# Kernel tuning notes

Measured on AMD Instinct MI355X. Metric: run time of the kernel, lower is better.

Reference implementation:

```python
import jax, jax.numpy as jnp
import numpy as np


def setup_inputs() -> dict:
    key = jax.random.key(0)
    kx, kr, kq, kk, kv = jax.random.split(key, 5)
    B, T, N, C = 4, 8, 2048, 128
    w_scale = 1.0 / np.sqrt(C)  # keep logits in a sane range
    return {
        "x": jax.random.normal(kx, (B, T, N, C), dtype=jnp.float32),
        "residual_source": jax.random.normal(kr, (B, N, C), dtype=jnp.float32),
        "Wq": jax.random.normal(kq, (C, C), dtype=jnp.float32) * w_scale,
        "Wk": jax.random.normal(kk, (C, C), dtype=jnp.float32) * w_scale,
        "Wv": jax.random.normal(kv, (C, C), dtype=jnp.float32) * w_scale,
    }


def reference(x, residual_source, Wq, Wk, Wv):
    # x: [B, T, N, C]; residual_source: [B, M, C] (expanded along T in the
    # original via unsqueeze+expand; here we exploit broadcasting instead of
    # materializing the [B, T, M, C] copy -- same math, k/v identical per T).
    q = jnp.einsum("btnc,cd->btnd", x, Wq)               # [B, T, N, D]
    k = jnp.einsum("bmc,cd->bmd", residual_source, Wk)   # [B, M, D]
    v = jnp.einsum("bmc,cd->bmd", residual_source, Wv)   # [B, M, D]
    # Unscaled attention, exactly as in the original (no 1/sqrt(d)).
    affinities = jnp.einsum("btnd,bmd->btnm", q, k)       # [B, T, N, M]
    attn = jax.nn.softmax(affinities, axis=-1)
    residual = jnp.einsum("btnm,bmd->btnd", attn, v)      # [B, T, N, D]
    return x + residual
```

## Files before the change

kernel.cpp:

```cpp
#include <hip/hip_runtime.h>


#define Bn 4
#define Tn 8
#define Nn 2048
#define Cn 128
#define Mn 2048
#define KVB 32
#define NT 64
#define QROWS 128
#define NQT (Nn / QROWS)

typedef __attribute__((ext_vector_type(4))) float f32x4;
typedef __attribute__((ext_vector_type(8))) _Float16 f16x8;
typedef __attribute__((address_space(3))) unsigned char lds_uc;
typedef const __attribute__((address_space(1))) unsigned char glb_uc;

__device__ __forceinline__ unsigned short f2h(float f) {
  _Float16 h = (_Float16)f;
  return __builtin_bit_cast(unsigned short, h);
}
__device__ __forceinline__ unsigned int pk2(float a, float b) {
  auto v = __builtin_amdgcn_cvt_pkrtz(a, b);
  return __builtin_bit_cast(unsigned int, v);
}
__device__ __forceinline__ f16x8 lds_read8(const unsigned char* base, int row,
                                           int colByte) {
  int byte = row * 256 + (colByte ^ ((row & 7) << 4));
  return *(const f16x8*)(base + byte);
}
__device__ __forceinline__ f16x8 lds_read8v(const unsigned char* base, int row,
                                            int colByte) {
  int byte = row * 64 + (colByte ^ ((row & 3) << 4));
  return *(const f16x8*)(base + byte);
}
__device__ __forceinline__ void gld16(const void* g, void* l) {
  __builtin_amdgcn_global_load_lds((glb_uc*)g, (lds_uc*)l, 16, 0, 0);
}

__global__ __launch_bounds__(256) void proj_kv_kernel(
    const float* __restrict__ rs, const float* __restrict__ Wk,
    const float* __restrict__ Wv, unsigned short* __restrict__ k_ws,
    unsigned short* __restrict__ vt_ws) {
  __shared__ unsigned char smem[48 * 1024];
  unsigned char* rsh = smem;
  unsigned char* wt = smem + 16 * 1024;

  const int bid = blockIdx.x;
  const int b = bid >> 5;
  const int kt64 = bid & 31;
  const int m0 = kt64 << 6;
  const int tid = threadIdx.x;
  const int wv = tid >> 6, lane = tid & 63;

  {
    const float4* g = (const float4*)(rs + ((size_t)b * Mn + m0) * Cn);
#pragma unroll
    for (int i = 0; i < 8; ++i) {
      int f = tid + i * 256;
      int row = f >> 5, c4 = f & 31;
      float4 v = g[f];
      int byte = row * 256 + ((c4 * 8) ^ ((row & 7) << 4));
      *(ushort4*)(rsh + byte) =
          make_ushort4(f2h(v.x), f2h(v.y), f2h(v.z), f2h(v.w));
    }
  }

#define STAGE_WT(Wp)                                                          \
  {                                                                           \
    const float4* g = (const float4*)(Wp);                                    \
    _Pragma("unroll") for (int i = 0; i < 16; ++i) {                          \
      int f = tid + i * 256;                                                  \
      int cc = f >> 5, d0 = (f & 31) * 4;                                     \
      float4 v = g[f];                                                        \
      float vv[4] = {v.x, v.y, v.z, v.w};                                     \
      _Pragma("unroll") for (int j = 0; j < 4; ++j) {                         \
        int row = d0 + j;                                                     \
        int byte = row * 256 + ((cc * 2) ^ ((row & 7) << 4));                 \
        *(unsigned short*)(wt + byte) = f2h(vv[j]);                           \
      }                                                                       \
    }                                                                         \
  }

  STAGE_WT(Wk);
  __syncthreads();

  const int arow = wv * 16 + (lane & 15);
  f16x8 ah[4];
#pragma unroll
  for (int ks = 0; ks < 4; ++ks)
    ah[ks] = lds_read8(rsh, arow, (lane >> 4) * 16 + ks * 64);

  f32x4 acc[8];
#pragma unroll
  for (int df = 0; df < 8; ++df) acc[df] = (f32x4)(0.0f);
#pragma unroll
  for (int ks = 0; ks < 4; ++ks)
#pragma unroll
    for (int df = 0; df < 8; ++df) {
      f16x8 bf = lds_read8(wt, df * 16 + (lane & 15), (lane >> 4) * 16 + ks * 64);
      acc[df] = __builtin_amdgcn_mfma_f32_16x16x32_f16(ah[ks], bf, acc[df], 0, 0, 0);
    }
  {
    unsigned char* kb = (unsigned char*)k_ws;
#pragma unroll
    for (int df = 0; df < 8; ++df)
#pragma unroll
      for (int r = 0; r < 4; ++r) {
        int row = wv * 16 + (lane >> 4) * 4 + r;
        int dcol = df * 16 + (lane & 15);
        size_t tile = (size_t)b * NT + (m0 >> 5) + (row >> 5);
        size_t byte = tile * 8192 + (row & 31) * 256 +
                      ((dcol * 2) ^ ((row & 7) << 4));
        *(unsigned short*)(kb + byte) = f2h(acc[df][r]);
      }
  }
  __syncthreads();

  STAGE_WT(Wv);
  __syncthreads();
#pragma unroll
  for (int df = 0; df < 8; ++df) acc[df] = (f32x4)(0.0f);
#pragma unroll
  for (int ks = 0; ks < 4; ++ks)
#pragma unroll
    for (int df = 0; df < 8; ++df) {
      f16x8 bf = lds_read8(wt, df * 16 + (lane & 15), (lane >> 4) * 16 + ks * 64);
      acc[df] = __builtin_amdgcn_mfma_f32_16x16x32_f16(ah[ks], bf, acc[df], 0, 0, 0);
    }
  {
    unsigned char* vb = (unsigned char*)vt_ws;
#pragma unroll
    for (int df = 0; df < 8; ++df)
#pragma unroll
      for (int r = 0; r < 4; ++r) {
        int row = wv * 16 + (lane >> 4) * 4 + r;
        int dcol = df * 16 + (lane & 15);
        size_t tile = (size_t)b * NT + (m0 >> 5) + (row >> 5);
        size_t byte = tile * 8192 + dcol * 64 +
                      (((row & 31) * 2) ^ ((dcol & 3) << 4));
        *(unsigned short*)(vb + byte) = f2h(acc[df][r]);
      }
  }
#undef STAGE_WT
}

__global__ __launch_bounds__(256, 2) void attn_kernel(
    const float* __restrict__ x, const float* __restrict__ Wq,
    const unsigned short* __restrict__ k_ws,
    const unsigned short* __restrict__ vt_ws, float* __restrict__ out) {
  __shared__ unsigned char smem[64 * 1024];

  const int bx = blockIdx.x;
  const int wb = ((bx & 7) << 6) | (bx >> 3);
  const int b = wb >> 7;
  const int t_ = (wb >> 4) & 7;
  const int n0 = (wb & 15) * QROWS;
  const int tid = threadIdx.x;
  const int wv = tid >> 6, lane = tid & 63;
  const int c = lane & 15, g = lane >> 4;

  const float* xg = x + (((size_t)b * Tn + t_) * Nn + n0) * Cn;
  unsigned char* xa = smem;
  unsigned char* wqb = smem + 32 * 1024;
  unsigned char* pb = smem + 48 * 1024 + wv * 2048;

  {
    const float4* gp = (const float4*)xg;
#pragma unroll
    for (int ii = 0; ii < 16; ++ii) {
      int f = tid + ii * 256;
      int row = f >> 5, c4 = f & 31;
      float4 v = gp[f];
      int byte = row * 256 + ((c4 * 8) ^ ((row & 7) << 4));
      *(ushort4*)(xa + byte) =
          make_ushort4(f2h(v.x), f2h(v.y), f2h(v.z), f2h(v.w));
    }
  }
  {
    const float4* gp = (const float4*)Wq;
#pragma unroll
    for (int ii = 0; ii < 16; ++ii) {
      int f = tid + ii * 256;
      int cc = f >> 5, d0 = (f & 31) * 4;
      float4 v = gp[f];
      float vv[4] = {v.x, v.y, v.z, v.w};
#pragma unroll
      for (int j = 0; j < 4; ++j) {
        int row = d0 + j;
        int byte = row * 256 + ((cc * 2) ^ ((row & 7) << 4));
        *(unsigned short*)(wqb + byte) = f2h(vv[j]);
      }
    }
  }
  __syncthreads();

  f32x4 qacc[2][8];
#pragma unroll
  for (int rb = 0; rb < 2; ++rb)
#pragma unroll
    for (int df = 0; df < 8; ++df) qacc[rb][df] = (f32x4)(0.0f);
  {
    f16x8 xf[2][4];
#pragma unroll
    for (int rb = 0; rb < 2; ++rb)
#pragma unroll
      for (int ks = 0; ks < 4; ++ks)
        xf[rb][ks] = lds_read8(xa, wv * 32 + rb * 16 + c, g * 16 + ks * 64);
#pragma unroll
    for (int ks = 0; ks < 4; ++ks)
#pragma unroll
      for (int df = 0; df < 8; ++df) {
        f16x8 bf = lds_read8(wqb, df * 16 + c, g * 16 + ks * 64);
        qacc[0][df] = __builtin_amdgcn_mfma_f32_16x16x32_f16(xf[0][ks], bf, qacc[0][df], 0, 0, 0);
        qacc[1][df] = __builtin_amdgcn_mfma_f32_16x16x32_f16(xf[1][ks], bf, qacc[1][df], 0, 0, 0);
      }
  }
  const float LOG2E = 1.4426950408889634f;
#pragma unroll
  for (int rb = 0; rb < 2; ++rb)
#pragma unroll
    for (int df = 0; df < 8; ++df)
#pragma unroll
      for (int r = 0; r < 4; ++r) {
        int row = wv * 32 + rb * 16 + g * 4 + r;
        int col = df * 16 + c;
        int byte = row * 256 + ((col * 2) ^ ((row & 7) << 4));
        *(unsigned short*)(xa + byte) = f2h(qacc[rb][df][r] * LOG2E);
      }
  f16x8 qf[2][4];
#pragma unroll
  for (int rb = 0; rb < 2; ++rb)
#pragma unroll
    for (int ks = 0; ks < 4; ++ks)
      qf[rb][ks] = lds_read8(xa, wv * 32 + rb * 16 + c, g * 16 + ks * 64);
  __syncthreads();

  f32x4 o[2][8];
#pragma unroll
  for (int rb = 0; rb < 2; ++rb)
#pragma unroll
    for (int df = 0; df < 8; ++df) o[rb][df] = (f32x4)(0.0f);
  float mrow[2] = {-INFINITY, -INFINITY};
  float lrow[2] = {0.f, 0.f};

  const unsigned char* khg = (const unsigned char*)k_ws + (size_t)b * NT * 8192;
  const unsigned char* vtg = (const unsigned char*)vt_ws + (size_t)b * NT * 8192;

  auto stageK = [&](int t) {
    const unsigned char* s = khg + (size_t)t * 8192 + tid * 16;
    unsigned char* d = smem + (t & 1) * 8192 + tid * 16;
    gld16(s, d);
    gld16(s + 4096, d + 4096);
  };
  auto stageV = [&](int t) {
    const unsigned char* s = vtg + (size_t)t * 8192 + tid * 16;
    unsigned char* d = smem + 16 * 1024 + (t & 3) * 8192 + tid * 16;
    gld16(s, d);
    gld16(s + 4096, d + 4096);
  };

  stageK(0);
  stageV(0);
  stageV(1);
  asm volatile("s_waitcnt vmcnt(2)" ::: "memory");
  __builtin_amdgcn_s_barrier();

  f16x8 pa[2];
#pragma unroll 1
  for (int t = 0; t < NT; ++t) {
    unsigned char* kb = smem + (t & 1) * 8192;
    unsigned char* vbp = smem + 16 * 1024 + ((t - 1) & 3) * 8192;

    f32x4 st[2][2];
#pragma unroll
    for (int rb = 0; rb < 2; ++rb)
#pragma unroll
      for (int kvb = 0; kvb < 2; ++kvb) st[rb][kvb] = (f32x4)(0.0f);
    __builtin_amdgcn_s_setprio(1);
#pragma unroll
    for (int ks = 0; ks < 4; ++ks)
#pragma unroll
      for (int kvb = 0; kvb < 2; ++kvb) {
        f16x8 kf = lds_read8(kb, kvb * 16 + c, g * 16 + ks * 64);
        st[0][kvb] = __builtin_amdgcn_mfma_f32_16x16x32_f16(kf, qf[0][ks], st[0][kvb], 0, 0, 0);
        st[1][kvb] = __builtin_amdgcn_mfma_f32_16x16x32_f16(kf, qf[1][ks], st[1][kvb], 0, 0, 0);
      }
    if (t > 0) {
#pragma unroll
      for (int df = 0; df < 8; ++df) {
        f16x8 vf = lds_read8v(vbp, df * 16 + c, g * 16);
        o[0][df] = __builtin_amdgcn_mfma_f32_16x16x32_f16(vf, pa[0], o[0][df], 0, 0, 0);
        o[1][df] = __builtin_amdgcn_mfma_f32_16x16x32_f16(vf, pa[1], o[1][df], 0, 0, 0);
      }
    }
    __builtin_amdgcn_s_setprio(0);

    if (t + 1 < NT) stageK(t + 1);
    if (t + 2 < NT) stageV(t + 2);

#pragma unroll
    for (int rb = 0; rb < 2; ++rb) {
      float tm = st[rb][0][0];
#pragma unroll
      for (int kvb = 0; kvb < 2; ++kvb)
#pragma unroll
        for (int r = 0; r < 4; ++r) tm = fmaxf(tm, st[rb][kvb][r]);
      if (__any(tm > mrow[rb] + 8.f)) {
        tm = fmaxf(tm, __shfl_xor(tm, 16));
        tm = fmaxf(tm, __shfl_xor(tm, 32));
        float newm = fmaxf(mrow[rb], tm);
        float scl = exp2f(mrow[rb] - newm);
#pragma unroll
        for (int df = 0; df < 8; ++df) o[rb][df] *= scl;
        lrow[rb] *= scl;
        mrow[rb] = newm;
      }
      float mn = mrow[rb];
      float ps = 0.f;
#pragma unroll
      for (int kvb = 0; kvb < 2; ++kvb) {
        float p0 = exp2f(st[rb][kvb][0] - mn);
        float p1 = exp2f(st[rb][kvb][1] - mn);
        float p2 = exp2f(st[rb][kvb][2] - mn);
        float p3 = exp2f(st[rb][kvb][3] - mn);
        ps += (p0 + p1) + (p2 + p3);
        int kv2 = kvb * 32 + g * 8;
        int base = rb * 1024 + c * 64;
        int swz = (c & 3) << 4;
        *(unsigned int*)(pb + base + (kv2 ^ swz)) = pk2(p0, p1);
        *(unsigned int*)(pb + base + ((kv2 + 4) ^ swz)) = pk2(p2, p3);
      }
      lrow[rb] += ps;
    }

    pa[0] = lds_read8v(pb, c, g * 16);
    pa[1] = lds_read8v(pb + 1024, c, g * 16);

    if (t < NT - 1) {
      if (t < NT - 2)
        asm volatile("s_waitcnt vmcnt(2)" ::: "memory");
      else
        asm volatile("s_waitcnt vmcnt(0)" ::: "memory");
      __builtin_amdgcn_s_barrier();
    }
  }
  {
    unsigned char* vbp = smem + 16 * 1024 + ((NT - 1) & 3) * 8192;
#pragma unroll
    for (int df = 0; df < 8; ++df) {
      f16x8 vf = lds_read8v(vbp, df * 16 + c, g * 16);
      o[0][df] = __builtin_amdgcn_mfma_f32_16x16x32_f16(vf, pa[0], o[0][df], 0, 0, 0);
      o[1][df] = __builtin_amdgcn_mfma_f32_16x16x32_f16(vf, pa[1], o[1][df], 0, 0, 0);
    }
  }
  __syncthreads();

#pragma unroll
  for (int rb = 0; rb < 2; ++rb) {
    lrow[rb] += __shfl_xor(lrow[rb], 16);
    lrow[rb] += __shfl_xor(lrow[rb], 32);
  }
  float inv[2] = {1.0f / lrow[0], 1.0f / lrow[1]};
#pragma unroll
  for (int rb = 0; rb < 2; ++rb)
#pragma unroll
    for (int df = 0; df < 8; ++df)
#pragma unroll
      for (int tq = 0; tq < 2; ++tq) {
        int d0 = df * 16 + g * 4 + tq * 2;
        int row = wv * 32 + rb * 16 + c;
        int byte = row * 256 + ((d0 * 2) ^ ((row & 7) << 4));
        *(unsigned int*)(smem + byte) =
            pk2(o[rb][df][2 * tq] * inv[rb], o[rb][df][2 * tq + 1] * inv[rb]);
      }
  __syncthreads();
  {
    const float4* xg4 = (const float4*)xg;
    float4* og4 = (float4*)(out + (((size_t)b * Tn + t_) * Nn + n0) * Cn);
#pragma unroll
    for (int ii = 0; ii < 8; ++ii) {
      int f = tid + ii * 256;
      int row = f >> 4, c16 = f & 15;
      int byte = row * 256 + ((c16 * 16) ^ ((row & 7) << 4));
      f16x8 v = *(const f16x8*)(smem + byte);
      float4 x0 = xg4[row * 32 + c16 * 2];
      float4 x1 = xg4[row * 32 + c16 * 2 + 1];
      og4[row * 32 + c16 * 2] =
          make_float4(x0.x + (float)v[0], x0.y + (float)v[1],
                      x0.z + (float)v[2], x0.w + (float)v[3]);
      og4[row * 32 + c16 * 2 + 1] =
          make_float4(x1.x + (float)v[4], x1.y + (float)v[5],
                      x1.z + (float)v[6], x1.w + (float)v[7]);
    }
  }
}

extern "C" void kernel_launch(void* const* d_in, const int* in_sizes, int n_in,
                              void* d_out, int out_size, void* d_ws,
                              size_t ws_size, hipStream_t stream) {
  const float* x = (const float*)d_in[0];
  const float* rs = (const float*)d_in[1];
  const float* Wq = (const float*)d_in[2];
  const float* Wk = (const float*)d_in[3];
  const float* Wv = (const float*)d_in[4];
  float* out = (float*)d_out;

  unsigned short* k_ws = (unsigned short*)d_ws;
  unsigned short* vt_ws = k_ws + (size_t)Bn * Mn * Cn;

  proj_kv_kernel<<<Bn * 32, 256, 0, stream>>>(rs, Wk, Wv, k_ws, vt_ws);
  attn_kernel<<<Bn * Tn * NQT, 256, 0, stream>>>(x, Wq, k_ws, vt_ws, out);
}
```

Baseline: 134.6 us.

## Split KV range across two wave groups with flash-decoding style merge

Attention blocks grow to 512 threads. Two groups of four waves each process half of every 64-row KV tile for the same 128 query rows, and their partial softmax states are merged through LDS at the end. The KV tile size doubles, K/V staging becomes a simple double buffer, and the V-transpose workspace layout changes to match. Wq is pre-scaled by log2e, and x is loaded straight into registers instead of being staged in LDS. This aims for more waves per CU and better latency hiding, at the cost of 80KB of LDS per block and extra merge work and barriers.

```diff
diff --git a/kernel.cpp b/kernel.cpp
--- a/kernel.cpp
+++ b/kernel.cpp
@@ -6,8 +6,8 @@
 #define Nn 2048
 #define Cn 128
 #define Mn 2048
-#define KVB 32
-#define NT 64
+#define KVB 64
+#define NT 32
 #define QROWS 128
 #define NQT (Nn / QROWS)
 
@@ -27,11 +27,6 @@
 __device__ __forceinline__ f16x8 lds_read8(const unsigned char* base, int row,
                                            int colByte) {
   int byte = row * 256 + (colByte ^ ((row & 7) << 4));
-  return *(const f16x8*)(base + byte);
-}
-__device__ __forceinline__ f16x8 lds_read8v(const unsigned char* base, int row,
-                                            int colByte) {
-  int byte = row * 64 + (colByte ^ ((row & 3) << 4));
   return *(const f16x8*)(base + byte);
 }
 __device__ __forceinline__ void gld16(const void* g, void* l) {
@@ -48,8 +43,8 @@
 
   const int bid = blockIdx.x;
   const int b = bid >> 5;
-  const int kt64 = bid & 31;
-  const int m0 = kt64 << 6;
+  const int kt = bid & 31;
+  const int m0 = kt << 6;
   const int tid = threadIdx.x;
   const int wv = tid >> 6, lane = tid & 63;
 
@@ -102,16 +97,15 @@
       acc[df] = __builtin_amdgcn_mfma_f32_16x16x32_f16(ah[ks], bf, acc[df], 0, 0, 0);
     }
   {
-    unsigned char* kb = (unsigned char*)k_ws;
+    unsigned char* kb =
+        (unsigned char*)k_ws + ((size_t)b * NT + kt) * 16384;
 #pragma unroll
     for (int df = 0; df < 8; ++df)
 #pragma unroll
       for (int r = 0; r < 4; ++r) {
         int row = wv * 16 + (lane >> 4) * 4 + r;
         int dcol = df * 16 + (lane & 15);
-        size_t tile = (size_t)b * NT + (m0 >> 5) + (row >> 5);
-        size_t byte = tile * 8192 + (row & 31) * 256 +
-                      ((dcol * 2) ^ ((row & 7) << 4));
+        int byte = row * 256 + ((dcol * 2) ^ ((row & 7) << 4));
         *(unsigned short*)(kb + byte) = f2h(acc[df][r]);
       }
   }
@@ -129,27 +123,27 @@
       acc[df] = __builtin_amdgcn_mfma_f32_16x16x32_f16(ah[ks], bf, acc[df], 0, 0, 0);
     }
   {
-    unsigned char* vb = (unsigned char*)vt_ws;
+    unsigned char* vb =
+        (unsigned char*)vt_ws + ((size_t)b * NT + kt) * 16384;
 #pragma unroll
     for (int df = 0; df < 8; ++df)
 #pragma unroll
       for (int r = 0; r < 4; ++r) {
         int row = wv * 16 + (lane >> 4) * 4 + r;
         int dcol = df * 16 + (lane & 15);
-        size_t tile = (size_t)b * NT + (m0 >> 5) + (row >> 5);
-        size_t byte = tile * 8192 + dcol * 64 +
-                      (((row & 31) * 2) ^ ((dcol & 3) << 4));
+        int byte = (dcol >> 1) * 256 +
+                   ((((dcol & 1) << 7) + row * 2) ^ (((dcol >> 1) & 7) << 4));
         *(unsigned short*)(vb + byte) = f2h(acc[df][r]);
       }
   }
 #undef STAGE_WT
 }
 
-__global__ __launch_bounds__(256, 2) void attn_kernel(
+__global__ __launch_bounds__(512, 4) void attn_kernel(
     const float* __restrict__ x, const float* __restrict__ Wq,
     const unsigned short* __restrict__ k_ws,
     const unsigned short* __restrict__ vt_ws, float* __restrict__ out) {
-  __shared__ unsigned char smem[64 * 1024];
+  __shared__ unsigned char smem[80 * 1024];
 
   const int bx = blockIdx.x;
   const int wb = ((bx & 7) << 6) | (bx >> 3);
@@ -158,30 +152,18 @@
   const int n0 = (wb & 15) * QROWS;
   const int tid = threadIdx.x;
   const int wv = tid >> 6, lane = tid & 63;
+  const int qg = wv & 3, kvg = wv >> 2;
   const int c = lane & 15, g = lane >> 4;
 
   const float* xg = x + (((size_t)b * Tn + t_) * Nn + n0) * Cn;
-  unsigned char* xa = smem;
-  unsigned char* wqb = smem + 32 * 1024;
-  unsigned char* pb = smem + 48 * 1024 + wv * 2048;
-
-  {
-    const float4* gp = (const float4*)xg;
-#pragma unroll
-    for (int ii = 0; ii < 16; ++ii) {
-      int f = tid + ii * 256;
-      int row = f >> 5, c4 = f & 31;
-      float4 v = gp[f];
-      int byte = row * 256 + ((c4 * 8) ^ ((row & 7) << 4));
-      *(ushort4*)(xa + byte) =
-          make_ushort4(f2h(v.x), f2h(v.y), f2h(v.z), f2h(v.w));
-    }
-  }
+  unsigned char* pbw = smem + 64 * 1024 + wv * 2048;
+
+  const float LOG2E = 1.4426950408889634f;
   {
     const float4* gp = (const float4*)Wq;
 #pragma unroll
-    for (int ii = 0; ii < 16; ++ii) {
-      int f = tid + ii * 256;
+    for (int ii = 0; ii < 8; ++ii) {
+      int f = tid + ii * 512;
       int cc = f >> 5, d0 = (f & 31) * 4;
       float4 v = gp[f];
       float vv[4] = {v.x, v.y, v.z, v.w};
@@ -189,7 +171,7 @@
       for (int j = 0; j < 4; ++j) {
         int row = d0 + j;
         int byte = row * 256 + ((cc * 2) ^ ((row & 7) << 4));
-        *(unsigned short*)(wqb + byte) = f2h(vv[j]);
+        *(unsigned short*)(smem + byte) = f2h(vv[j] * LOG2E);
       }
     }
   }
@@ -203,37 +185,51 @@
   {
     f16x8 xf[2][4];
 #pragma unroll
-    for (int rb = 0; rb < 2; ++rb)
-#pragma unroll
-      for (int ks = 0; ks < 4; ++ks)
-        xf[rb][ks] = lds_read8(xa, wv * 32 + rb * 16 + c, g * 16 + ks * 64);
+    for (int rb = 0; rb < 2; ++rb) {
+      const float* xrow = xg + (size_t)(qg * 32 + rb * 16 + c) * Cn;
+#pragma unroll
+      for (int ks = 0; ks < 4; ++ks) {
+        int d0 = ks * 32 + g * 8;
+        float4 a = *(const float4*)(xrow + d0);
+        float4 b2 = *(const float4*)(xrow + d0 + 4);
+        f16x8 h;
+        h[0] = (_Float16)a.x; h[1] = (_Float16)a.y;
+        h[2] = (_Float16)a.z; h[3] = (_Float16)a.w;
+        h[4] = (_Float16)b2.x; h[5] = (_Float16)b2.y;
+        h[6] = (_Float16)b2.z; h[7] = (_Float16)b2.w;
+        xf[rb][ks] = h;
+      }
+    }
 #pragma unroll
     for (int ks = 0; ks < 4; ++ks)
 #pragma unroll
       for (int df = 0; df < 8; ++df) {
-        f16x8 bf = lds_read8(wqb, df * 16 + c, g * 16 + ks * 64);
+        f16x8 bf = lds_read8(smem, df * 16 + c, g * 16 + ks * 64);
         qacc[0][df] = __builtin_amdgcn_mfma_f32_16x16x32_f16(xf[0][ks], bf, qacc[0][df], 0, 0, 0);
         qacc[1][df] = __builtin_amdgcn_mfma_f32_16x16x32_f16(xf[1][ks], bf, qacc[1][df], 0, 0, 0);
       }
   }
-  const float LOG2E = 1.4426950408889634f;
+  __syncthreads();
+  if (kvg == 0) {
+#pragma unroll
+    for (int rb = 0; rb < 2; ++rb)
+#pragma unroll
+      for (int df = 0; df < 8; ++df)
+#pragma unroll
+        for (int r = 0; r < 4; ++r) {
+          int row = qg * 32 + rb * 16 + g * 4 + r;
+          int dq = df * 16 + c;
+          int byte = row * 256 + ((dq * 2) ^ ((row & 7) << 4));
+          *(unsigned short*)(smem + byte) = f2h(qacc[rb][df][r]);
+        }
+  }
+  __syncthreads();
+  f16x8 qf[2][4];
 #pragma unroll
   for (int rb = 0; rb < 2; ++rb)
 #pragma unroll
-    for (int df = 0; df < 8; ++df)
-#pragma unroll
-      for (int r = 0; r < 4; ++r) {
-        int row = wv * 32 + rb * 16 + g * 4 + r;
-        int col = df * 16 + c;
-        int byte = row * 256 + ((col * 2) ^ ((row & 7) << 4));
-        *(unsigned short*)(xa + byte) = f2h(qacc[rb][df][r] * LOG2E);
-      }
-  f16x8 qf[2][4];
-#pragma unroll
-  for (int rb = 0; rb < 2; ++rb)
-#pragma unroll
     for (int ks = 0; ks < 4; ++ks)
-      qf[rb][ks] = lds_read8(xa, wv * 32 + rb * 16 + c, g * 16 + ks * 64);
+      qf[rb][ks] = lds_read8(smem, qg * 32 + rb * 16 + c, g * 16 + ks * 64);
   __syncthreads();
 
   f32x4 o[2][8];
@@ -244,33 +240,28 @@
   float mrow[2] = {-INFINITY, -INFINITY};
   float lrow[2] = {0.f, 0.f};
 
-  const unsigned char* khg = (const unsigned char*)k_ws + (size_t)b * NT * 8192;
-  const unsigned char* vtg = (const unsigned char*)vt_ws + (size_t)b * NT * 8192;
-
-  auto stageK = [&](int t) {
-    const unsigned char* s = khg + (size_t)t * 8192 + tid * 16;
-    unsigned char* d = smem + (t & 1) * 8192 + tid * 16;
-    gld16(s, d);
-    gld16(s + 4096, d + 4096);
+  const unsigned char* khg = (const unsigned char*)k_ws + (size_t)b * NT * 16384;
+  const unsigned char* vtg = (const unsigned char*)vt_ws + (size_t)b * NT * 16384;
+
+  auto stage = [&](int t) {
+    unsigned char* kd = smem + (t & 1) * 16384 + tid * 16;
+    unsigned char* vd = smem + 32 * 1024 + (t & 1) * 16384 + tid * 16;
+    const unsigned char* ks_ = khg + (size_t)t * 16384 + tid * 16;
+    const unsigned char* vs = vtg + (size_t)t * 16384 + tid * 16;
+    gld16(ks_, kd);
+    gld16(ks_ + 8192, kd + 8192);
+    gld16(vs, vd);
+    gld16(vs + 8192, vd + 8192);
   };
-  auto stageV = [&](int t) {
-    const unsigned char* s = vtg + (size_t)t * 8192 + tid * 16;
-    unsigned char* d = smem + 16 * 1024 + (t & 3) * 8192 + tid * 16;
-    gld16(s, d);
-    gld16(s + 4096, d + 4096);
-  };
-
-  stageK(0);
-  stageV(0);
-  stageV(1);
-  asm volatile("s_waitcnt vmcnt(2)" ::: "memory");
-  __builtin_amdgcn_s_barrier();
-
-  f16x8 pa[2];
+
+  stage(0);
+  __syncthreads();
+
 #pragma unroll 1
   for (int t = 0; t < NT; ++t) {
-    unsigned char* kb = smem + (t & 1) * 8192;
-    unsigned char* vbp = smem + 16 * 1024 + ((t - 1) & 3) * 8192;
+    unsigned char* kb = smem + (t & 1) * 16384;
+    unsigned char* vb = smem + 32 * 1024 + (t & 1) * 16384;
+    if (t + 1 < NT) stage(t + 1);
 
     f32x4 st[2][2];
 #pragma unroll
@@ -282,30 +273,18 @@
     for (int ks = 0; ks < 4; ++ks)
 #pragma unroll
       for (int kvb = 0; kvb < 2; ++kvb) {
-        f16x8 kf = lds_read8(kb, kvb * 16 + c, g * 16 + ks * 64);
+        f16x8 kf = lds_read8(kb, kvg * 32 + kvb * 16 + c, g * 16 + ks * 64);
         st[0][kvb] = __builtin_amdgcn_mfma_f32_16x16x32_f16(kf, qf[0][ks], st[0][kvb], 0, 0, 0);
         st[1][kvb] = __builtin_amdgcn_mfma_f32_16x16x32_f16(kf, qf[1][ks], st[1][kvb], 0, 0, 0);
       }
-    if (t > 0) {
-#pragma unroll
-      for (int df = 0; df < 8; ++df) {
-        f16x8 vf = lds_read8v(vbp, df * 16 + c, g * 16);
-        o[0][df] = __builtin_amdgcn_mfma_f32_16x16x32_f16(vf, pa[0], o[0][df], 0, 0, 0);
-        o[1][df] = __builtin_amdgcn_mfma_f32_16x16x32_f16(vf, pa[1], o[1][df], 0, 0, 0);
-      }
-    }
     __builtin_amdgcn_s_setprio(0);
 
-    if (t + 1 < NT) stageK(t + 1);
-    if (t + 2 < NT) stageV(t + 2);
-
 #pragma unroll
     for (int rb = 0; rb < 2; ++rb) {
-      float tm = st[rb][0][0];
-#pragma unroll
-      for (int kvb = 0; kvb < 2; ++kvb)
-#pragma unroll
-        for (int r = 0; r < 4; ++r) tm = fmaxf(tm, st[rb][kvb][r]);
+      float tm = fmaxf(fmaxf(fmaxf(st[rb][0][0], st[rb][0][1]),
+                             fmaxf(st[rb][0][2], st[rb][0][3])),
+                       fmaxf(fmaxf(st[rb][1][0], st[rb][1][1]),
+                             fmaxf(st[rb][1][2], st[rb][1][3])));
       if (__any(tm > mrow[rb] + 8.f)) {
         tm = fmaxf(tm, __shfl_xor(tm, 16));
         tm = fmaxf(tm, __shfl_xor(tm, 32));
@@ -325,64 +304,105 @@
         float p2 = exp2f(st[rb][kvb][2] - mn);
         float p3 = exp2f(st[rb][kvb][3] - mn);
         ps += (p0 + p1) + (p2 + p3);
+        int row = rb * 16 + c;
         int kv2 = kvb * 32 + g * 8;
-        int base = rb * 1024 + c * 64;
         int swz = (c & 3) << 4;
-        *(unsigned int*)(pb + base + (kv2 ^ swz)) = pk2(p0, p1);
-        *(unsigned int*)(pb + base + ((kv2 + 4) ^ swz)) = pk2(p2, p3);
+        *(unsigned int*)(pbw + row * 64 + (kv2 ^ swz)) = pk2(p0, p1);
+        *(unsigned int*)(pbw + row * 64 + ((kv2 + 4) ^ swz)) = pk2(p2, p3);
       }
       lrow[rb] += ps;
     }
 
-    pa[0] = lds_read8v(pb, c, g * 16);
-    pa[1] = lds_read8v(pb + 1024, c, g * 16);
-
-    if (t < NT - 1) {
-      if (t < NT - 2)
-        asm volatile("s_waitcnt vmcnt(2)" ::: "memory");
-      else
-        asm volatile("s_waitcnt vmcnt(0)" ::: "memory");
-      __builtin_amdgcn_s_barrier();
-    }
-  }
-  {
-    unsigned char* vbp = smem + 16 * 1024 + ((NT - 1) & 3) * 8192;
+    f16x8 pa[2];
+#pragma unroll
+    for (int rb = 0; rb < 2; ++rb) {
+      int row = rb * 16 + c;
+      pa[rb] = *(const f16x8*)(pbw + row * 64 + ((g * 16) ^ ((c & 3) << 4)));
+    }
+
+    __builtin_amdgcn_s_setprio(1);
 #pragma unroll
     for (int df = 0; df < 8; ++df) {
-      f16x8 vf = lds_read8v(vbp, df * 16 + c, g * 16);
+      int srow = df * 8 + (c >> 1);
+      int byte = srow * 256 +
+                 ((((c & 1) << 7) | (kvg * 64 + g * 16)) ^ ((srow & 7) << 4));
+      f16x8 vf = *(const f16x8*)(vb + byte);
       o[0][df] = __builtin_amdgcn_mfma_f32_16x16x32_f16(vf, pa[0], o[0][df], 0, 0, 0);
       o[1][df] = __builtin_amdgcn_mfma_f32_16x16x32_f16(vf, pa[1], o[1][df], 0, 0, 0);
     }
-  }
-  __syncthreads();
+    __builtin_amdgcn_s_setprio(0);
+    __syncthreads();
+  }
 
 #pragma unroll
   for (int rb = 0; rb < 2; ++rb) {
     lrow[rb] += __shfl_xor(lrow[rb], 16);
     lrow[rb] += __shfl_xor(lrow[rb], 32);
   }
-  float inv[2] = {1.0f / lrow[0], 1.0f / lrow[1]};
-#pragma unroll
-  for (int rb = 0; rb < 2; ++rb)
-#pragma unroll
-    for (int df = 0; df < 8; ++df)
-#pragma unroll
-      for (int tq = 0; tq < 2; ++tq) {
-        int d0 = df * 16 + g * 4 + tq * 2;
-        int row = wv * 32 + rb * 16 + c;
-        int byte = row * 256 + ((d0 * 2) ^ ((row & 7) << 4));
-        *(unsigned int*)(smem + byte) =
-            pk2(o[rb][df][2 * tq] * inv[rb], o[rb][df][2 * tq + 1] * inv[rb]);
-      }
+  float* ML = (float*)(smem + 64 * 1024);
+  if (g == 0) {
+#pragma unroll
+    for (int rb = 0; rb < 2; ++rb) {
+      ML[((wv * 2 + rb) * 16 + c) * 2 + 0] = mrow[rb];
+      ML[((wv * 2 + rb) * 16 + c) * 2 + 1] = lrow[rb];
+    }
+  }
+  __syncthreads();
+  const int pw = wv ^ 4;
+  float coef[2];
+#pragma unroll
+  for (int rb = 0; rb < 2; ++rb) {
+    float mp = ML[((pw * 2 + rb) * 16 + c) * 2 + 0];
+    float lp = ML[((pw * 2 + rb) * 16 + c) * 2 + 1];
+    float m12 = fmaxf(mrow[rb], mp);
+    float s0 = exp2f(mrow[rb] - m12);
+    float sp = exp2f(mp - m12);
+    float ltot = lrow[rb] * s0 + lp * sp;
+    coef[rb] = s0 / ltot;
+  }
+  __syncthreads();
+  if (kvg == 1) {
+#pragma unroll
+    for (int rb = 0; rb < 2; ++rb)
+#pragma unroll
+      for (int df = 0; df < 8; ++df)
+#pragma unroll
+        for (int h = 0; h < 2; ++h) {
+          int row = qg * 32 + rb * 16 + c;
+          int d0 = df * 16 + g * 4 + 2 * h;
+          int byte = row * 256 + ((d0 * 2) ^ ((row & 7) << 4));
+          *(unsigned int*)(smem + byte) =
+              pk2(o[rb][df][2 * h] * coef[rb], o[rb][df][2 * h + 1] * coef[rb]);
+        }
+  }
+  __syncthreads();
+  if (kvg == 0) {
+#pragma unroll
+    for (int rb = 0; rb < 2; ++rb)
+#pragma unroll
+      for (int df = 0; df < 8; ++df)
+#pragma unroll
+        for (int h = 0; h < 2; ++h) {
+          int row = qg * 32 + rb * 16 + c;
+          int d0 = df * 16 + g * 4 + 2 * h;
+          int sw = (d0 * 2) ^ ((row & 7) << 4);
+          unsigned int v = *(const unsigned int*)(smem + row * 256 + sw);
+          float plo = (float)__builtin_bit_cast(_Float16, (unsigned short)(v & 0xffffu));
+          float phi = (float)__builtin_bit_cast(_Float16, (unsigned short)(v >> 16));
+          float r0 = o[rb][df][2 * h] * coef[rb] + plo;
+          float r1 = o[rb][df][2 * h + 1] * coef[rb] + phi;
+          *(unsigned int*)(smem + 32 * 1024 + row * 256 + sw) = pk2(r0, r1);
+        }
+  }
   __syncthreads();
   {
     const float4* xg4 = (const float4*)xg;
     float4* og4 = (float4*)(out + (((size_t)b * Tn + t_) * Nn + n0) * Cn);
 #pragma unroll
-    for (int ii = 0; ii < 8; ++ii) {
-      int f = tid + ii * 256;
+    for (int ii = 0; ii < 4; ++ii) {
+      int f = tid + ii * 512;
       int row = f >> 4, c16 = f & 15;
-      int byte = row * 256 + ((c16 * 16) ^ ((row & 7) << 4));
+      int byte = 32 * 1024 + row * 256 + ((c16 * 16) ^ ((row & 7) << 4));
       f16x8 v = *(const f16x8*)(smem + byte);
       float4 x0 = xg4[row * 32 + c16 * 2];
       float4 x1 = xg4[row * 32 + c16 * 2 + 1];
@@ -409,6 +429,6 @@
   unsigned short* k_ws = (unsigned short*)d_ws;
   unsigned short* vt_ws = k_ws + (size_t)Bn * Mn * Cn;
 
-  proj_kv_kernel<<<Bn * 32, 256, 0, stream>>>(rs, Wk, Wv, k_ws, vt_ws);
-  attn_kernel<<<Bn * Tn * NQT, 256, 0, stream>>>(x, Wq, k_ws, vt_ws, out);
-}
+  proj_kv_kernel<<<Bn * NT, 256, 0, stream>>>(rs, Wk, Wv, k_ws, vt_ws);
+  attn_kernel<<<Bn * Tn * NQT, 512, 0, stream>>>(x, Wq, k_ws, vt_ws, out);
+}
```

Result: slower. 156.7 us (+16.4%).
